# Kernel tuning notes

Hardware: AMD Instinct MI355X
Metric: run time of the kernel (lower is better)

Reference implementation:

```python
import jax, jax.numpy as jnp
import numpy as np

SCALE_FACTOR = 1.0
VIS_MAX = 1024


def setup_inputs() -> dict:
    key = jax.random.key(0)
    kq, kk, kv = jax.random.split(key, 3)
    B, C, H, W = 4, 256, 64, 64
    Q = jax.random.normal(kq, (B, C, H, W), dtype=jnp.float32)
    K = jax.random.normal(kk, (B, C, H, W), dtype=jnp.float32)
    V = jax.random.normal(kv, (B, C, H, W), dtype=jnp.float32)
    return {"Q": Q, "K": K, "V": V}


def reference(Q, K, V):
    # Q,K: [B,C,H,W] -> flatten spatial dims to HW
    B, C, H, W = Q.shape
    HW = H * W
    Q_flat = Q.reshape(B, C, HW).transpose(0, 2, 1)  # [B, HW, C]
    K_flat = K.reshape(B, C, HW)                      # [B, C, HW]
    # Full scaled score matrix [B, HW, HW]; argmax over keys reproduces the
    # chunked running-max/argmax (strict '>' update keeps first max, matching
    # jnp.argmax tie-breaking).
    S = jnp.einsum('bqc,bck->bqk', Q_flat, K_flat) * SCALE_FACTOR
    H_idx = jnp.argmax(S, axis=2).astype(jnp.int64)   # [B, HW]
    vis = min(VIS_MAX, HW)
    S_vis = S[:, :vis, :vis]                          # [B, vis, vis]
    return S_vis, H_idx
```

## Files before the change

### kernel.cpp

```cpp
#include <hip/hip_runtime.h>
#include <stdint.h>

#define B_   4
#define C_   256
#define HW_  4096
#define VIS_ 1024
#define NKT  16

using half8   = __attribute__((ext_vector_type(8))) _Float16;
using floatx4 = __attribute__((ext_vector_type(4))) float;

__device__ __forceinline__ unsigned mapf(float v) {
    unsigned u = __float_as_uint(v);
    return (u & 0x80000000u) ? ~u : (u | 0x80000000u);
}

__global__ void init_ws_kernel(unsigned long long* ws, int n) {
    int i = blockIdx.x * blockDim.x + threadIdx.x;
    if (i < n) ws[i] = 0ull;
}

__global__ void finalize_kernel(const unsigned long long* __restrict__ ws,
                                float* __restrict__ out1, int n, int slices) {
    int i = blockIdx.x * blockDim.x + threadIdx.x;
    if (i < n) {
        unsigned long long best = ws[i];
        for (int k = 1; k < slices; ++k) {
            unsigned long long v = ws[(size_t)k * n + i];
            if (v > best) best = v;
        }
        unsigned kinv = (unsigned)(best & 0xFFFFFFFFull);
        out1[i] = (float)(HW_ - 1 - (int)kinv);
    }
}


#define BARRIER __builtin_amdgcn_s_barrier()
#define LGKM0   asm volatile("s_waitcnt lgkmcnt(0)" ::: "memory")
#define SCHEDB  __builtin_amdgcn_sched_barrier(0)

__device__ __forceinline__ void stage_load(const float* __restrict__ Qp,
                                           const float* __restrict__ Kp,
                                           int kb, int t,
                                           float (&ra)[2][8], float (&rb)[2][8])
{
    const int hw = t & 255, o0 = t >> 8;
    #pragma unroll
    for (int k = 0; k < 2; ++k) {
        const int c0 = kb + (o0 + 2 * k) * 8;
        const float* qa = Qp + (size_t)c0 * HW_ + hw;
        const float* ka = Kp + (size_t)c0 * HW_ + hw;
        #pragma unroll
        for (int j = 0; j < 8; ++j) {
            ra[k][j] = qa[(size_t)j * HW_];
            rb[k][j] = ka[(size_t)j * HW_];
        }
    }
}

__device__ __forceinline__ void cvt_write(_Float16* lds, int p, int t,
                                          const float (&ra)[2][8],
                                          const float (&rb)[2][8])
{
    _Float16* Ah = lds + (p * 4 + 0) * 8192;
    _Float16* Al = lds + (p * 4 + 1) * 8192;
    _Float16* Bh = lds + (p * 4 + 2) * 8192;
    _Float16* Bl = lds + (p * 4 + 3) * 8192;
    const int hw = t & 255, o0 = t >> 8, swz = (hw >> 1) & 3;
    #pragma unroll
    for (int k = 0; k < 2; ++k) {
        const int ch = (o0 + 2 * k) ^ swz;
        half8 ha, la, hb, lb;
        #pragma unroll
        for (int j = 0; j < 8; ++j) {
            float v = ra[k][j];
            _Float16 h = (_Float16)v;
            ha[j] = h; la[j] = (_Float16)(v - (float)h);
            float w = rb[k][j];
            _Float16 g = (_Float16)w;
            hb[j] = g; lb[j] = (_Float16)(w - (float)g);
        }
        *(half8*)(Ah + hw * 32 + ch * 8) = ha;
        *(half8*)(Al + hw * 32 + ch * 8) = la;
        *(half8*)(Bh + hw * 32 + ch * 8) = hb;
        *(half8*)(Bl + hw * 32 + ch * 8) = lb;
    }
}

template<int MQ>
__device__ __forceinline__ void ds_load_a(const _Float16* base, int wave_m, int s,
                                          int quad, half8 (&a)[4]) {
    #pragma unroll
    for (int mi = 0; mi < 4; ++mi) {
        int row = wave_m * 128 + MQ * 64 + mi * 16 + s;
        int ch  = quad ^ ((row >> 1) & 3);
        a[mi] = *(const half8*)(base + row * 32 + ch * 8);
    }
}

__device__ __forceinline__ void ds_load_b(const _Float16* base, int wave_n, int s,
                                          int quad, half8 (&bfr)[4]) {
    #pragma unroll
    for (int ni = 0; ni < 4; ++ni) {
        int col = wave_n * 64 + ni * 16 + s;
        int ch  = quad ^ ((col >> 1) & 3);
        bfr[ni] = *(const half8*)(base + col * 32 + ch * 8);
    }
}

template<int MQ>
__device__ __forceinline__ void do_mfma(const half8 (&a)[4], const half8 (&bfr)[4],
                                        floatx4 (&acc)[8][4]) {
    __builtin_amdgcn_s_setprio(1);
    #pragma unroll
    for (int mi = 0; mi < 4; ++mi)
        #pragma unroll
        for (int ni = 0; ni < 4; ++ni)
            acc[MQ * 4 + mi][ni] = __builtin_amdgcn_mfma_f32_16x16x32_f16(
                a[mi], bfr[ni], acc[MQ * 4 + mi][ni], 0, 0, 0);
    __builtin_amdgcn_s_setprio(0);
}

__device__ __forceinline__ void chunk_compute(const _Float16* lds, int p,
    int wave_m, int wave_n, int s, int quad, floatx4 (&acc)[8][4])
{
    const _Float16* Ah = lds + (p * 4 + 0) * 8192;
    const _Float16* Al = lds + (p * 4 + 1) * 8192;
    const _Float16* Bh = lds + (p * 4 + 2) * 8192;
    const _Float16* Bl = lds + (p * 4 + 3) * 8192;
    half8 bh[4], bl[4], a[4];
    ds_load_b(Bh, wave_n, s, quad, bh);
    ds_load_b(Bl, wave_n, s, quad, bl);
    ds_load_a<0>(Ah, wave_m, s, quad, a);
    do_mfma<0>(a, bh, acc);
    do_mfma<0>(a, bl, acc);
    ds_load_a<1>(Ah, wave_m, s, quad, a);
    do_mfma<1>(a, bh, acc);
    do_mfma<1>(a, bl, acc);
    ds_load_a<0>(Al, wave_m, s, quad, a);
    do_mfma<0>(a, bh, acc);
    ds_load_a<1>(Al, wave_m, s, quad, a);
    do_mfma<1>(a, bh, acc);
}

__global__ __launch_bounds__(512, 2) void gemm_mfma_kernel(
    const float* __restrict__ Q, const float* __restrict__ K,
    float* __restrict__ out0, unsigned long long* __restrict__ keys_part)
{
    __shared__ __align__(16) _Float16 lds[65536];

    const int t      = threadIdx.x;
    const int lane   = t & 63;
    const int wave   = t >> 6;
    const int quad   = lane >> 4;
    const int s      = lane & 15;
    const int wave_m = wave >> 2;
    const int wave_n = wave & 3;

    const int n    = blockIdx.x;
    const int wgid = (n & 7) * 128 + (n >> 3);
    const int kt   = wgid & 15;
    const int qt   = (wgid >> 4) & 15;
    const int b    = wgid >> 8;

    const float* Qp = Q + (size_t)b * C_ * HW_ + qt * 256;
    const float* Kp = K + (size_t)b * C_ * HW_ + kt * 256;

    float ra[2][8], rb[2][8];

    stage_load(Qp, Kp, 0, t, ra, rb);
    cvt_write(lds, 0, t, ra, rb);
    stage_load(Qp, Kp, 32, t, ra, rb);
    cvt_write(lds, 1, t, ra, rb);
    stage_load(Qp, Kp, 64, t, ra, rb);
    LGKM0; BARRIER; SCHEDB;

    floatx4 acc[8][4] = {};

    #pragma unroll 1
    for (int c = 0; c < 6; ++c) {
        chunk_compute(lds, c & 1, wave_m, wave_n, s, quad, acc);
        LGKM0; BARRIER;
        cvt_write(lds, c & 1, t, ra, rb);
        if (c < 5) stage_load(Qp, Kp, (c + 3) * 32, t, ra, rb);
        LGKM0; BARRIER; SCHEDB;
    }
    chunk_compute(lds, 0, wave_m, wave_n, s, quad, acc);
    chunk_compute(lds, 1, wave_m, wave_n, s, quad, acc);

    if (qt < 4 && kt < 4) {
        #pragma unroll
        for (int mi8 = 0; mi8 < 8; ++mi8)
            #pragma unroll
            for (int r = 0; r < 4; ++r) {
                int grow = qt * 256 + wave_m * 128 + mi8 * 16 + quad * 4 + r;
                float* orow = out0 + ((size_t)b * VIS_ + grow) * VIS_ + kt * 256 + wave_n * 64;
                #pragma unroll
                for (int ni = 0; ni < 4; ++ni)
                    orow[ni * 16 + s] = acc[mi8][ni][r];
            }
    }

    __syncthreads();
    unsigned long long* red = (unsigned long long*)lds;

    #pragma unroll
    for (int mi8 = 0; mi8 < 8; ++mi8) {
        #pragma unroll
        for (int r = 0; r < 4; ++r) {
            float best = acc[mi8][0][r];
            int bcol = wave_n * 64 + s;
            #pragma unroll
            for (int ni = 1; ni < 4; ++ni) {
                float v = acc[mi8][ni][r];
                if (v > best) { best = v; bcol = wave_n * 64 + ni * 16 + s; }
            }
            int gcol = kt * 256 + bcol;
            unsigned long long key = ((unsigned long long)mapf(best) << 32)
                                   | (unsigned)(HW_ - 1 - gcol);
            #pragma unroll
            for (int m = 1; m < 16; m <<= 1) {
                unsigned long long o = __shfl_xor(key, m, 64);
                if (o > key) key = o;
            }
            if (s == 0)
                red[(wave_m * 128 + mi8 * 16 + quad * 4 + r) * 4 + wave_n] = key;
        }
    }
    __syncthreads();
    if (t < 256) {
        const unsigned long long* rr = red + t * 4;
        unsigned long long k0 = rr[0], k1 = rr[1], k2 = rr[2], k3 = rr[3];
        unsigned long long m01 = k0 > k1 ? k0 : k1;
        unsigned long long m23 = k2 > k3 ? k2 : k3;
        unsigned long long m = m01 > m23 ? m01 : m23;
        keys_part[(size_t)kt * (B_ * HW_) + (size_t)b * HW_ + qt * 256 + t] = m;
    }
}

#define BT   64
#define BK   32
#define LDP  68

__global__ __launch_bounds__(256) void gemm_argmax_kernel(
    const float* __restrict__ Q, const float* __restrict__ K,
    float* __restrict__ out0, unsigned long long* __restrict__ ws)
{
    __shared__ float As[BK][LDP];
    __shared__ float Bs[BK][LDP];
    __shared__ unsigned long long red[BT][17];

    const int t  = threadIdx.x;
    const int tx = t & 15;
    const int ty = t >> 4;
    const int k0 = blockIdx.x * BT;
    const int q0 = blockIdx.y * BT;
    const int b  = blockIdx.z;

    const float* Qb = Q + (size_t)b * C_ * HW_;
    const float* Kb = K + (size_t)b * C_ * HW_;

    float acc[4][4] = {{0.f},{0.f},{0.f},{0.f}};

    for (int c0 = 0; c0 < C_; c0 += BK) {
        #pragma unroll
        for (int i = 0; i < 2; ++i) {
            int idx = i * 256 + t;
            int row = idx >> 4;
            int col = (idx & 15) * 4;
            const float4 a  = *(const float4*)(Qb + (size_t)(c0 + row) * HW_ + q0 + col);
            const float4 bv = *(const float4*)(Kb + (size_t)(c0 + row) * HW_ + k0 + col);
            *(float4*)(&As[row][col]) = a;
            *(float4*)(&Bs[row][col]) = bv;
        }
        __syncthreads();
        #pragma unroll
        for (int cc = 0; cc < BK; ++cc) {
            const float4 av = *(const float4*)(&As[cc][ty * 4]);
            const float4 bv = *(const float4*)(&Bs[cc][tx * 4]);
            const float a_[4] = {av.x, av.y, av.z, av.w};
            const float b_[4] = {bv.x, bv.y, bv.z, bv.w};
            #pragma unroll
            for (int i = 0; i < 4; ++i)
                #pragma unroll
                for (int j = 0; j < 4; ++j)
                    acc[i][j] = fmaf(a_[i], b_[j], acc[i][j]);
        }
        __syncthreads();
    }

    if (q0 < VIS_ && k0 < VIS_) {
        #pragma unroll
        for (int i = 0; i < 4; ++i) {
            float4 v = make_float4(acc[i][0], acc[i][1], acc[i][2], acc[i][3]);
            size_t off = (size_t)b * VIS_ * VIS_ + (size_t)(q0 + ty * 4 + i) * VIS_ + (k0 + tx * 4);
            *(float4*)(out0 + off) = v;
        }
    }

    #pragma unroll
    for (int i = 0; i < 4; ++i) {
        float best = acc[i][0];
        int   bj   = 0;
        #pragma unroll
        for (int j = 1; j < 4; ++j)
            if (acc[i][j] > best) { best = acc[i][j]; bj = j; }
        int kidx = k0 + tx * 4 + bj;
        unsigned long long key = ((unsigned long long)mapf(best) << 32)
                               | (unsigned)(HW_ - 1 - kidx);
        red[ty * 4 + i][tx] = key;
    }
    __syncthreads();
    if (t < BT) {
        unsigned long long best = red[t][0];
        #pragma unroll
        for (int j = 1; j < 16; ++j) {
            unsigned long long v = red[t][j];
            if (v > best) best = v;
        }
        atomicMax(&ws[(size_t)b * HW_ + q0 + t], best);
    }
}

extern "C" void kernel_launch(void* const* d_in, const int* in_sizes, int n_in,
                              void* d_out, int out_size, void* d_ws, size_t ws_size,
                              hipStream_t stream) {
    const float* Q = (const float*)d_in[0];
    const float* K = (const float*)d_in[1];
    float* out0 = (float*)d_out;
    float* out1 = out0 + (size_t)B_ * VIS_ * VIS_;

    unsigned long long* keys = (unsigned long long*)d_ws;
    const int n = B_ * HW_;
    const size_t part_bytes = (size_t)NKT * n * 8;

    if (ws_size >= part_bytes) {
        gemm_mfma_kernel<<<dim3((HW_ / 256) * (HW_ / 256) * B_), 512, 0, stream>>>(Q, K, out0, keys);
        finalize_kernel<<<(n + 255) / 256, 256, 0, stream>>>(keys, out1, n, NKT);
    } else {
        init_ws_kernel<<<(n + 255) / 256, 256, 0, stream>>>(keys, n);
        gemm_argmax_kernel<<<dim3(HW_ / BT, HW_ / BT, B_), 256, 0, stream>>>(Q, K, out0, keys);
        finalize_kernel<<<(n + 255) / 256, 256, 0, stream>>>(keys, out1, n, 1);
    }
}
```

Measured before the change: 204.2 us.

## Use 1024-thread workgroups with 4x4 wave grid and 64-row wave tiles

```diff
diff --git a/kernel.cpp b/kernel.cpp
--- a/kernel.cpp
+++ b/kernel.cpp
@@ -42,120 +42,107 @@
 __device__ __forceinline__ void stage_load(const float* __restrict__ Qp,
                                            const float* __restrict__ Kp,
                                            int kb, int t,
-                                           float (&ra)[2][8], float (&rb)[2][8])
-{
-    const int hw = t & 255, o0 = t >> 8;
-    #pragma unroll
-    for (int k = 0; k < 2; ++k) {
-        const int c0 = kb + (o0 + 2 * k) * 8;
-        const float* qa = Qp + (size_t)c0 * HW_ + hw;
-        const float* ka = Kp + (size_t)c0 * HW_ + hw;
-        #pragma unroll
-        for (int j = 0; j < 8; ++j) {
-            ra[k][j] = qa[(size_t)j * HW_];
-            rb[k][j] = ka[(size_t)j * HW_];
-        }
+                                           float (&ra)[8], float (&rb)[8])
+{
+    const int hw = t & 255, o = t >> 8;
+    const int c0 = kb + o * 8;
+    const float* qa = Qp + (size_t)c0 * HW_ + hw;
+    const float* ka = Kp + (size_t)c0 * HW_ + hw;
+    #pragma unroll
+    for (int j = 0; j < 8; ++j) {
+        ra[j] = qa[(size_t)j * HW_];
+        rb[j] = ka[(size_t)j * HW_];
     }
 }
 
 __device__ __forceinline__ void cvt_write(_Float16* lds, int p, int t,
-                                          const float (&ra)[2][8],
-                                          const float (&rb)[2][8])
+                                          const float (&ra)[8],
+                                          const float (&rb)[8])
 {
     _Float16* Ah = lds + (p * 4 + 0) * 8192;
     _Float16* Al = lds + (p * 4 + 1) * 8192;
     _Float16* Bh = lds + (p * 4 + 2) * 8192;
     _Float16* Bl = lds + (p * 4 + 3) * 8192;
-    const int hw = t & 255, o0 = t >> 8, swz = (hw >> 1) & 3;
-    #pragma unroll
-    for (int k = 0; k < 2; ++k) {
-        const int ch = (o0 + 2 * k) ^ swz;
-        half8 ha, la, hb, lb;
-        #pragma unroll
-        for (int j = 0; j < 8; ++j) {
-            float v = ra[k][j];
-            _Float16 h = (_Float16)v;
-            ha[j] = h; la[j] = (_Float16)(v - (float)h);
-            float w = rb[k][j];
-            _Float16 g = (_Float16)w;
-            hb[j] = g; lb[j] = (_Float16)(w - (float)g);
-        }
-        *(half8*)(Ah + hw * 32 + ch * 8) = ha;
-        *(half8*)(Al + hw * 32 + ch * 8) = la;
-        *(half8*)(Bh + hw * 32 + ch * 8) = hb;
-        *(half8*)(Bl + hw * 32 + ch * 8) = lb;
-    }
-}
-
-template<int MQ>
-__device__ __forceinline__ void ds_load_a(const _Float16* base, int wave_m, int s,
+    const int hw = t & 255, o = t >> 8;
+    const int ch = o ^ ((hw >> 1) & 3);
+    half8 ha, la, hb, lb;
+    #pragma unroll
+    for (int j = 0; j < 8; ++j) {
+        float v = ra[j];
+        _Float16 h = (_Float16)v;
+        ha[j] = h; la[j] = (_Float16)(v - (float)h);
+        float w = rb[j];
+        _Float16 g = (_Float16)w;
+        hb[j] = g; lb[j] = (_Float16)(w - (float)g);
+    }
+    *(half8*)(Ah + hw * 32 + ch * 8) = ha;
+    *(half8*)(Al + hw * 32 + ch * 8) = la;
+    *(half8*)(Bh + hw * 32 + ch * 8) = hb;
+    *(half8*)(Bl + hw * 32 + ch * 8) = lb;
+}
+
+__device__ __forceinline__ void ds_load_a(const _Float16* base, int wm, int s,
                                           int quad, half8 (&a)[4]) {
     #pragma unroll
     for (int mi = 0; mi < 4; ++mi) {
-        int row = wave_m * 128 + MQ * 64 + mi * 16 + s;
+        int row = wm * 64 + mi * 16 + s;
         int ch  = quad ^ ((row >> 1) & 3);
         a[mi] = *(const half8*)(base + row * 32 + ch * 8);
     }
 }
 
-__device__ __forceinline__ void ds_load_b(const _Float16* base, int wave_n, int s,
+__device__ __forceinline__ void ds_load_b(const _Float16* base, int wn, int s,
                                           int quad, half8 (&bfr)[4]) {
     #pragma unroll
     for (int ni = 0; ni < 4; ++ni) {
-        int col = wave_n * 64 + ni * 16 + s;
+        int col = wn * 64 + ni * 16 + s;
         int ch  = quad ^ ((col >> 1) & 3);
         bfr[ni] = *(const half8*)(base + col * 32 + ch * 8);
     }
 }
 
-template<int MQ>
 __device__ __forceinline__ void do_mfma(const half8 (&a)[4], const half8 (&bfr)[4],
-                                        floatx4 (&acc)[8][4]) {
+                                        floatx4 (&acc)[4][4]) {
     __builtin_amdgcn_s_setprio(1);
     #pragma unroll
     for (int mi = 0; mi < 4; ++mi)
         #pragma unroll
         for (int ni = 0; ni < 4; ++ni)
-            acc[MQ * 4 + mi][ni] = __builtin_amdgcn_mfma_f32_16x16x32_f16(
-                a[mi], bfr[ni], acc[MQ * 4 + mi][ni], 0, 0, 0);
+            acc[mi][ni] = __builtin_amdgcn_mfma_f32_16x16x32_f16(
+                a[mi], bfr[ni], acc[mi][ni], 0, 0, 0);
     __builtin_amdgcn_s_setprio(0);
 }
 
 __device__ __forceinline__ void chunk_compute(const _Float16* lds, int p,
-    int wave_m, int wave_n, int s, int quad, floatx4 (&acc)[8][4])
+    int wm, int wn, int s, int quad, floatx4 (&acc)[4][4])
 {
     const _Float16* Ah = lds + (p * 4 + 0) * 8192;
     const _Float16* Al = lds + (p * 4 + 1) * 8192;
     const _Float16* Bh = lds + (p * 4 + 2) * 8192;
     const _Float16* Bl = lds + (p * 4 + 3) * 8192;
     half8 bh[4], bl[4], a[4];
-    ds_load_b(Bh, wave_n, s, quad, bh);
-    ds_load_b(Bl, wave_n, s, quad, bl);
-    ds_load_a<0>(Ah, wave_m, s, quad, a);
-    do_mfma<0>(a, bh, acc);
-    do_mfma<0>(a, bl, acc);
-    ds_load_a<1>(Ah, wave_m, s, quad, a);
-    do_mfma<1>(a, bh, acc);
-    do_mfma<1>(a, bl, acc);
-    ds_load_a<0>(Al, wave_m, s, quad, a);
-    do_mfma<0>(a, bh, acc);
-    ds_load_a<1>(Al, wave_m, s, quad, a);
-    do_mfma<1>(a, bh, acc);
-}
-
-__global__ __launch_bounds__(512, 2) void gemm_mfma_kernel(
+    ds_load_b(Bh, wn, s, quad, bh);
+    ds_load_b(Bl, wn, s, quad, bl);
+    ds_load_a(Ah, wm, s, quad, a);
+    do_mfma(a, bh, acc);
+    do_mfma(a, bl, acc);
+    ds_load_a(Al, wm, s, quad, a);
+    do_mfma(a, bh, acc);
+}
+
+__global__ __launch_bounds__(1024, 1) void gemm_mfma_kernel(
     const float* __restrict__ Q, const float* __restrict__ K,
     float* __restrict__ out0, unsigned long long* __restrict__ keys_part)
 {
     __shared__ __align__(16) _Float16 lds[65536];
 
-    const int t      = threadIdx.x;
-    const int lane   = t & 63;
-    const int wave   = t >> 6;
-    const int quad   = lane >> 4;
-    const int s      = lane & 15;
-    const int wave_m = wave >> 2;
-    const int wave_n = wave & 3;
+    const int t    = threadIdx.x;
+    const int lane = t & 63;
+    const int wave = t >> 6;
+    const int quad = lane >> 4;
+    const int s    = lane & 15;
+    const int wm   = wave >> 2;
+    const int wn   = wave & 3;
 
     const int n    = blockIdx.x;
     const int wgid = (n & 7) * 128 + (n >> 3);
@@ -166,38 +153,37 @@
     const float* Qp = Q + (size_t)b * C_ * HW_ + qt * 256;
     const float* Kp = K + (size_t)b * C_ * HW_ + kt * 256;
 
-    float ra[2][8], rb[2][8];
+    float ra[8], rb[8];
 
     stage_load(Qp, Kp, 0, t, ra, rb);
     cvt_write(lds, 0, t, ra, rb);
     stage_load(Qp, Kp, 32, t, ra, rb);
     cvt_write(lds, 1, t, ra, rb);
-    stage_load(Qp, Kp, 64, t, ra, rb);
     LGKM0; BARRIER; SCHEDB;
 
-    floatx4 acc[8][4] = {};
+    floatx4 acc[4][4] = {};
 
     #pragma unroll 1
     for (int c = 0; c < 6; ++c) {
-        chunk_compute(lds, c & 1, wave_m, wave_n, s, quad, acc);
+        chunk_compute(lds, c & 1, wm, wn, s, quad, acc);
         LGKM0; BARRIER;
+        stage_load(Qp, Kp, (c + 2) * 32, t, ra, rb);
         cvt_write(lds, c & 1, t, ra, rb);
-        if (c < 5) stage_load(Qp, Kp, (c + 3) * 32, t, ra, rb);
         LGKM0; BARRIER; SCHEDB;
     }
-    chunk_compute(lds, 0, wave_m, wave_n, s, quad, acc);
-    chunk_compute(lds, 1, wave_m, wave_n, s, quad, acc);
+    chunk_compute(lds, 0, wm, wn, s, quad, acc);
+    chunk_compute(lds, 1, wm, wn, s, quad, acc);
 
     if (qt < 4 && kt < 4) {
         #pragma unroll
-        for (int mi8 = 0; mi8 < 8; ++mi8)
+        for (int mi = 0; mi < 4; ++mi)
             #pragma unroll
             for (int r = 0; r < 4; ++r) {
-                int grow = qt * 256 + wave_m * 128 + mi8 * 16 + quad * 4 + r;
-                float* orow = out0 + ((size_t)b * VIS_ + grow) * VIS_ + kt * 256 + wave_n * 64;
+                int grow = qt * 256 + wm * 64 + mi * 16 + quad * 4 + r;
+                float* orow = out0 + ((size_t)b * VIS_ + grow) * VIS_ + kt * 256 + wn * 64;
                 #pragma unroll
                 for (int ni = 0; ni < 4; ++ni)
-                    orow[ni * 16 + s] = acc[mi8][ni][r];
+                    orow[ni * 16 + s] = acc[mi][ni][r];
             }
     }
 
@@ -205,15 +191,15 @@
     unsigned long long* red = (unsigned long long*)lds;
 
     #pragma unroll
-    for (int mi8 = 0; mi8 < 8; ++mi8) {
+    for (int mi = 0; mi < 4; ++mi) {
         #pragma unroll
         for (int r = 0; r < 4; ++r) {
-            float best = acc[mi8][0][r];
-            int bcol = wave_n * 64 + s;
+            float best = acc[mi][0][r];
+            int bcol = wn * 64 + s;
             #pragma unroll
             for (int ni = 1; ni < 4; ++ni) {
-                float v = acc[mi8][ni][r];
-                if (v > best) { best = v; bcol = wave_n * 64 + ni * 16 + s; }
+                float v = acc[mi][ni][r];
+                if (v > best) { best = v; bcol = wn * 64 + ni * 16 + s; }
             }
             int gcol = kt * 256 + bcol;
             unsigned long long key = ((unsigned long long)mapf(best) << 32)
@@ -224,7 +210,7 @@
                 if (o > key) key = o;
             }
             if (s == 0)
-                red[(wave_m * 128 + mi8 * 16 + quad * 4 + r) * 4 + wave_n] = key;
+                red[(wm * 64 + mi * 16 + quad * 4 + r) * 4 + wn] = key;
         }
     }
     __syncthreads();
@@ -335,7 +321,7 @@
     const size_t part_bytes = (size_t)NKT * n * 8;
 
     if (ws_size >= part_bytes) {
-        gemm_mfma_kernel<<<dim3((HW_ / 256) * (HW_ / 256) * B_), 512, 0, stream>>>(Q, K, out0, keys);
+        gemm_mfma_kernel<<<dim3((HW_ / 256) * (HW_ / 256) * B_), 1024, 0, stream>>>(Q, K, out0, keys);
         finalize_kernel<<<(n + 255) / 256, 256, 0, stream>>>(keys, out1, n, NKT);
     } else {
         init_ws_kernel<<<(n + 255) / 256, 256, 0, stream>>>(keys, n);
```

Measured after the change: 196.4 us. 3.8% less time.
